# Optimization experiments

Measured on AMD Instinct MI355X. Metric: run time of the kernel, lower is better.

The kernel has to match this reference:

```python
import jax, jax.numpy as jnp
import numpy as np
from jax.scipy.special import gammaln, logsumexp

# Model dims (match init_kwargs)
N1, N2, N3 = 16, 16, 8          # n_state_list
S = N1 * N2 * N3                # tot_dim = 2048 flattened states
M = 16                          # m_dimensions
T = 16384                       # T_max


def setup_inputs() -> dict:
    key = jax.random.key(0)
    ks = jax.random.split(key, 10)
    # observed Poisson counts, shape (T, M)
    x = jax.random.randint(ks[0], (T, M), 0, 20)
    # per-factor Poisson rates: lambda_list[i] = exp(randn(N_i, M)) as in __init__
    lam1 = jnp.exp(jax.random.normal(ks[1], (N1, M), dtype=jnp.float32))
    lam2 = jnp.exp(jax.random.normal(ks[2], (N2, M), dtype=jnp.float32))
    lam3 = jnp.exp(jax.random.normal(ks[3], (N3, M), dtype=jnp.float32))
    # per-factor log transition matrices: softmax over dim 0 (A[next, prev] columns sum to 1)
    logA1 = jax.nn.log_softmax(jax.random.normal(ks[4], (N1, N1), dtype=jnp.float32), axis=0)
    logA2 = jax.nn.log_softmax(jax.random.normal(ks[5], (N2, N2), dtype=jnp.float32), axis=0)
    logA3 = jax.nn.log_softmax(jax.random.normal(ks[6], (N3, N3), dtype=jnp.float32), axis=0)
    # per-factor log state priors: log_softmax(rand(N)*10)
    logpi1 = jax.nn.log_softmax(jax.random.uniform(ks[7], (N1,), dtype=jnp.float32) * 10.0)
    logpi2 = jax.nn.log_softmax(jax.random.uniform(ks[8], (N2,), dtype=jnp.float32) * 10.0)
    logpi3 = jax.nn.log_softmax(jax.random.uniform(ks[9], (N3,), dtype=jnp.float32) * 10.0)
    return {"x": x, "lam1": lam1, "lam2": lam2, "lam3": lam3,
            "logA1": logA1, "logA2": logA2, "logA3": logA3,
            "logpi1": logpi1, "logpi2": logpi2, "logpi3": logpi3}


def reference(x, lam1, lam2, lam3, logA1, logA2, logA3, logpi1, logpi2, logpi3):
    # combine_lambdas: lam_c[s1,s2,s3,m] = lam1[s1,m] + lam2[s2,m] + lam3[s3,m]
    lam_c = (lam1[:, None, None, :] + lam2[None, :, None, :]
             + lam3[None, None, :, :]).reshape(S, M)  # (S, M)
    xf = x.astype(jnp.float32)
    # Poisson log-pmf summed over the M observation dims:
    # em[t, s] = sum_m x[t,m]*log(lam_c[s,m]) - lam_c[s,m] - lgamma(x[t,m]+1)
    em = (xf @ jnp.log(lam_c).T
          - lam_c.sum(axis=-1)[None, :]
          - gammaln(xf + 1.0).sum(axis=-1)[:, None])  # (T, S)
    # combined log transition: logA[dest_flat, prev_flat] = sum_i logA_i[d_i, p_i]
    logA = (logA1[:, None, None, :, None, None]
            + logA2[None, :, None, None, :, None]
            + logA3[None, None, :, None, None, :]).reshape(S, S)
    # combined log priors
    logpi = (logpi1[:, None, None] + logpi2[None, :, None]
             + logpi3[None, None, :]).reshape(S)
    # log-domain forward recurrence (log_alpha_calc)
    alpha0 = em[0] + logpi
    def step(prev, em_t):
        a = em_t + logsumexp(logA + prev[None, :], axis=1)
        return a, None
    alpha_last, _ = jax.lax.scan(step, alpha0, em[1:])
    # log p(x) = logsumexp over final-step alpha
    return logsumexp(alpha_last)
```

## Files before the change

kernel.cpp:

```cpp
#include <hip/hip_runtime.h>
#include <math.h>

#define TMAX 16384
#define MDIM 16
#define SD   2048
#define CLEN 16
#define WUP  8
#define CHKB 512
#define NS   (CLEN + WUP - 1)
#define EROWS 32

typedef unsigned int  uint;
typedef unsigned short ushort;
typedef __attribute__((ext_vector_type(8))) short short8;
typedef __attribute__((ext_vector_type(4))) short short4v;
typedef __attribute__((ext_vector_type(4))) float floatx4;
typedef __attribute__((ext_vector_type(2))) uint uintx2;

template<int CTRL>
__device__ __forceinline__ float fmax_dpp(float v) {
    int o = __builtin_amdgcn_update_dpp(__float_as_int(v), __float_as_int(v),
                                        CTRL, 0xf, 0xf, false);
    return fmaxf(v, __int_as_float(o));
}
__device__ __forceinline__ float waveMax64(float v) {
    v = fmax_dpp<0x111>(v);
    v = fmax_dpp<0x112>(v);
    v = fmax_dpp<0x114>(v);
    v = fmax_dpp<0x118>(v);
    v = fmax_dpp<0x142>(v);
    v = fmax_dpp<0x143>(v);
    return __int_as_float(__builtin_amdgcn_readlane(__float_as_int(v), 63));
}
__device__ __forceinline__ float waveSumF(float v) {
    #pragma unroll
    for (int o = 32; o > 0; o >>= 1) v += __shfl_xor(v, o, 64);
    return v;
}
__device__ __forceinline__ double waveSumD(double v) {
    #pragma unroll
    for (int o = 32; o > 0; o >>= 1) v += __shfl_xor(v, o, 64);
    return v;
}

__device__ __forceinline__ short f2bfs(float f) {
    uint u = __float_as_uint(f);
    return (short)((u + 0x7FFFu + ((u >> 16) & 1u)) >> 16);
}
__device__ __forceinline__ uint pkbf(float a, float b) {
    uint ua = __float_as_uint(a), ub = __float_as_uint(b);
    ua = (ua + 0x7FFFu + ((ua >> 16) & 1u)) >> 16;
    ub = (ub + 0x7FFFu + ((ub >> 16) & 1u)) & 0xFFFF0000u;
    return ua | ub;
}
__device__ __forceinline__ short4v pk4(float a, float b, float c, float d) {
    short4v r;
    r[0] = f2bfs(a); r[1] = f2bfs(b); r[2] = f2bfs(c); r[3] = f2bfs(d);
    return r;
}
__device__ __forceinline__ float bfl(uint u) { return __uint_as_float(u << 16); }
__device__ __forceinline__ float bfh(uint u) { return __uint_as_float(u & 0xFFFF0000u); }

#if __has_builtin(__builtin_amdgcn_mfma_f32_16x16x16bf16_1k)
#define MFMA16(a, b, c) __builtin_amdgcn_mfma_f32_16x16x16bf16_1k(a, b, c, 0, 0, 0)
#else
__device__ __forceinline__ floatx4 mfma16_asm(short4v a, short4v b, floatx4 c) {
    asm volatile("v_mfma_f32_16x16x16_bf16 %0, %1, %2, %0\n\t"
                 "s_nop 7\n\ts_nop 7"
                 : "+v"(c) : "v"(a), "v"(b));
    return c;
}
#define MFMA16(a, b, c) mfma16_asm(a, b, c)
#endif
#define MFMA32(a, b, c) __builtin_amdgcn_mfma_f32_16x16x32_bf16(a, b, c, 0, 0, 0)

__global__ __launch_bounds__(512, 2)
void emP_kernel(const int* __restrict__ x,
                const float* __restrict__ lam1,
                const float* __restrict__ lam2,
                const float* __restrict__ lam3,
                ushort* __restrict__ P,
                float* __restrict__ SumAuxArr,
                float* __restrict__ out) {
    __shared__ float wmx[EROWS][8];
    __shared__ float DemS[EROWS];
    __shared__ float lgtbl[32];
    __shared__ __align__(16) float xfs[EROWS * MDIM];
    __shared__ float lgred;
    const int tid = threadIdx.x, lane = tid & 63, wv = tid >> 6;
    const int q = lane >> 4, nn = lane & 15;
    const int d2 = 2 * wv + (nn >> 3);
    const int d3 = nn & 7;

    if (tid < 32) lgtbl[tid] = lgammaf((float)tid + 1.0f);
    if (tid == 0) lgred = 0.f;

    float llc[4][16], ls[4];
    #pragma unroll
    for (int j = 0; j < 4; ++j) {
        const int d1 = 4 * q + j;
        float sum = 0.f;
        #pragma unroll
        for (int m = 0; m < 16; ++m) {
            float la = lam1[d1 * 16 + m] + lam2[d2 * 16 + m] + lam3[d3 * 16 + m];
            sum += la;
            llc[j][m] = __logf(la);
        }
        ls[j] = sum;
    }

    const int t0 = blockIdx.x * EROWS;
    const int xv = x[t0 * MDIM + tid];
    xfs[tid] = (float)xv;
    __syncthreads();
    {
        double lg = (double)lgtbl[xv & 31];
        lg = waveSumD(lg);
        if (lane == 0) atomicAdd(&lgred, (float)lg);
    }

    float em[EROWS][4];
    #pragma unroll
    for (int ti = 0; ti < EROWS; ++ti) {
        float xr[16];
        *(float4*)&xr[0]  = *(const float4*)&xfs[ti * 16 + 0];
        *(float4*)&xr[4]  = *(const float4*)&xfs[ti * 16 + 4];
        *(float4*)&xr[8]  = *(const float4*)&xfs[ti * 16 + 8];
        *(float4*)&xr[12] = *(const float4*)&xfs[ti * 16 + 12];
        float vm = -3.4e38f;
        #pragma unroll
        for (int j = 0; j < 4; ++j) {
            float d = 0.f;
            #pragma unroll
            for (int m = 0; m < 16; ++m) d = fmaf(xr[m], llc[j][m], d);
            em[ti][j] = d - ls[j];
            vm = fmaxf(vm, em[ti][j]);
        }
        vm = waveMax64(vm);
        if (lane == 0) wmx[ti][wv] = vm;
    }
    __syncthreads();
    if (tid < 32) {
        float m = wmx[tid][0];
        #pragma unroll
        for (int i = 1; i < 8; ++i) m = fmaxf(m, wmx[tid][i]);
        DemS[tid] = m;
    }
    __syncthreads();

    #pragma unroll
    for (int ti = 0; ti < EROWS; ++ti) {
        const float Dem = DemS[ti];
        uint2 w;
        w.x = pkbf(__expf(em[ti][0] - Dem), __expf(em[ti][1] - Dem));
        w.y = pkbf(__expf(em[ti][2] - Dem), __expf(em[ti][3] - Dem));
        *(uint2*)(P + (size_t)(t0 + ti) * SD + tid * 4) = w;
    }

    if (tid == 0) {
        double sumD = 0.0;
        #pragma unroll
        for (int i = 0; i < EROWS; ++i) sumD += (double)DemS[i];
        SumAuxArr[blockIdx.x] = (float)sumD - lgred;
        if (blockIdx.x == 0) out[0] = 0.f;
    }
}

__global__ __launch_bounds__(512, 4)
void fhmm_chunk_kernel(const ushort* __restrict__ P,
                       const float* __restrict__ SumAuxArr,
                       const float* __restrict__ logA1,
                       const float* __restrict__ logA2,
                       const float* __restrict__ logA3,
                       const float* __restrict__ logpi1,
                       const float* __restrict__ logpi2,
                       const float* __restrict__ logpi3,
                       float* __restrict__ out)
{
    __shared__ __align__(16) short c1bA[2 * 2048];
    __shared__ __align__(16) short c1bB[2 * 2048];
    __shared__ float wmAA[8], wmAB[8];
    __shared__ float sred[8];
    __shared__ float saux8[8];

    const int tid  = threadIdx.x;
    const int lane = tid & 63;
    const int wv   = tid >> 6;
    const int q    = lane >> 4;
    const int ml   = lane & 15;

    const int b   = blockIdx.x;
    const int tA0 = (b == 0) ? 0 : 32 * b - WUP;
    const int tB0 = 32 * b + (CLEN - WUP);

    short4v bA1k;
    #pragma unroll
    for (int j = 0; j < 4; ++j)
        bA1k[j] = f2bfs(__expf(logA1[ml * 16 + 4 * q + j]));

    const int d2p = 2 * wv + (ml >> 3);
    const int d3p = ml & 7;
    short8 bK[4];
    #pragma unroll
    for (int jc = 0; jc < 4; ++jc)
        #pragma unroll
        for (int i = 0; i < 8; ++i)
            bK[jc][i] = f2bfs(__expf(logA2[d2p * 16 + 4 * jc + q] + logA3[d3p * 8 + i]));

    const int oS1w = ml * 128 + ((((2 * wv + (q >> 1)) ^ ml) & 15) << 3) + 4 * (q & 1);
    int o23[4];
    #pragma unroll
    for (int jc = 0; jc < 4; ++jc)
        o23[jc] = ml * 128 + ((((4 * jc + q) ^ ml) & 15) << 3);

    if (b == 0) {
        float sx = waveSumF(SumAuxArr[tid]);
        if (lane == 0) saux8[wv] = sx;
    }

    double OFF = 0.0;
    float nuA[4], nuB[4];
    {
        uintx2 p0 = *(const uintx2*)(P + (size_t)tA0 * SD + tid * 4);
        if (b == 0) {
            float lp23 = logpi2[d2p] + logpi3[d3p];
            nuA[0] = bfl(p0.x) * __expf(logpi1[4 * q + 0] + lp23);
            nuA[1] = bfh(p0.x) * __expf(logpi1[4 * q + 1] + lp23);
            nuA[2] = bfl(p0.y) * __expf(logpi1[4 * q + 2] + lp23);
            nuA[3] = bfh(p0.y) * __expf(logpi1[4 * q + 3] + lp23);
        } else {
            nuA[0] = bfl(p0.x); nuA[1] = bfh(p0.x);
            nuA[2] = bfl(p0.y); nuA[3] = bfh(p0.y);
        }
    }
    {
        uintx2 p0 = *(const uintx2*)(P + (size_t)tB0 * SD + tid * 4);
        nuB[0] = bfl(p0.x); nuB[1] = bfh(p0.x);
        nuB[2] = bfl(p0.y); nuB[3] = bfh(p0.y);
    }

    uintx2 PbA0 = *(const uintx2*)(P + (size_t)(tA0 + 1) * SD + tid * 4);
    uintx2 PbA1 = *(const uintx2*)(P + (size_t)(tA0 + 2) * SD + tid * 4);
    uintx2 PbB0 = *(const uintx2*)(P + (size_t)(tB0 + 1) * SD + tid * 4);
    uintx2 PbB1 = *(const uintx2*)(P + (size_t)(tB0 + 2) * SD + tid * 4);

#define SSTEP(S, RESC, ACCFA, ACCFB)                                            \
{                                                                               \
    const int par = (S) & 1;          \
    short* cAq = c1bA + (par << 11);                                            \
    short* cBq = c1bB + (par << 11);                                            \
    {                                 \
        short4v afA = pk4(nuA[0], nuA[1], nuA[2], nuA[3]);                      \
        short4v afB = pk4(nuB[0], nuB[1], nuB[2], nuB[3]);                      \
        floatx4 sA = {0.f, 0.f, 0.f, 0.f};                                      \
        floatx4 sB = {0.f, 0.f, 0.f, 0.f};                                      \
        sA = MFMA16(afA, bA1k, sA);                                             \
        sB = MFMA16(afB, bA1k, sB);                                             \
        ((uintx2*)(cAq + oS1w))[0] = (uintx2){pkbf(sA[0], sA[1]), pkbf(sA[2], sA[3])}; \
        ((uintx2*)(cBq + oS1w))[0] = (uintx2){pkbf(sB[0], sB[1]), pkbf(sB[2], sB[3])}; \
    }                                                                           \
    __syncthreads();                                                            \
    const int tnA = (tA0 + (S) + 2 < TMAX) ? tA0 + (S) + 2 : TMAX - 1;          \
    const int tnB = (tB0 + (S) + 2 < TMAX) ? tB0 + (S) + 2 : TMAX - 1;          \
    uintx2 PbA2 = *(const uintx2*)(P + (size_t)tnA * SD + tid * 4);             \
    uintx2 PbB2 = *(const uintx2*)(P + (size_t)tnB * SD + tid * 4);             \
    float invA = 1.f, invB = 1.f;                                               \
    if (RESC) {                                                                 \
        float mpA = waveMax64(wmAA[lane & 7]);                                  \
        float mpB = waveMax64(wmAB[lane & 7]);                                  \
        float mgA = fmaxf(mpA, 1e-30f);                                         \
        float mgB = fmaxf(mpB, 1e-30f);                                         \
        invA = __builtin_amdgcn_rcpf(mgA);                                      \
        invB = __builtin_amdgcn_rcpf(mgB);                                      \
        if (tid == 0) {                                                         \
            if (ACCFA) OFF += (double)__logf(mgA);                              \
            if (ACCFB) OFF += (double)__logf(mgB);                              \
        }                                                                       \
    }                                                                           \
    {              \
        short8 fA0 = *(const short8*)(cAq + o23[0]);                            \
        short8 fA1 = *(const short8*)(cAq + o23[1]);                            \
        short8 fA2 = *(const short8*)(cAq + o23[2]);                            \
        short8 fA3 = *(const short8*)(cAq + o23[3]);                            \
        short8 fB0 = *(const short8*)(cBq + o23[0]);                            \
        short8 fB1 = *(const short8*)(cBq + o23[1]);                            \
        short8 fB2 = *(const short8*)(cBq + o23[2]);                            \
        short8 fB3 = *(const short8*)(cBq + o23[3]);                            \
        floatx4 aA0 = {0.f, 0.f, 0.f, 0.f};                                     \
        floatx4 aA1 = {0.f, 0.f, 0.f, 0.f};                                     \
        floatx4 aB0 = {0.f, 0.f, 0.f, 0.f};                                     \
        floatx4 aB1 = {0.f, 0.f, 0.f, 0.f};                                     \
        aA0 = MFMA32(fA0, bK[0], aA0);  aB0 = MFMA32(fB0, bK[0], aB0);          \
        aA1 = MFMA32(fA1, bK[1], aA1);  aB1 = MFMA32(fB1, bK[1], aB1);          \
        aA0 = MFMA32(fA2, bK[2], aA0);  aB0 = MFMA32(fB2, bK[2], aB0);          \
        aA1 = MFMA32(fA3, bK[3], aA1);  aB1 = MFMA32(fB3, bK[3], aB1);          \
        floatx4 accA = aA0 + aA1;                                               \
        floatx4 accB = aB0 + aB1;                                               \
        if (RESC) {                                                             \
            nuA[0] = bfl(PbA0.x) * accA[0] * invA;                              \
            nuA[1] = bfh(PbA0.x) * accA[1] * invA;                              \
            nuA[2] = bfl(PbA0.y) * accA[2] * invA;                              \
            nuA[3] = bfh(PbA0.y) * accA[3] * invA;                              \
            nuB[0] = bfl(PbB0.x) * accB[0] * invB;                              \
            nuB[1] = bfh(PbB0.x) * accB[1] * invB;                              \
            nuB[2] = bfl(PbB0.y) * accB[2] * invB;                              \
            nuB[3] = bfh(PbB0.y) * accB[3] * invB;                              \
        } else {                                                                \
            nuA[0] = bfl(PbA0.x) * accA[0];                                     \
            nuA[1] = bfh(PbA0.x) * accA[1];                                     \
            nuA[2] = bfl(PbA0.y) * accA[2];                                     \
            nuA[3] = bfh(PbA0.y) * accA[3];                                     \
            nuB[0] = bfl(PbB0.x) * accB[0];                                     \
            nuB[1] = bfh(PbB0.x) * accB[1];                                     \
            nuB[2] = bfl(PbB0.y) * accB[2];                                     \
            nuB[3] = bfh(PbB0.y) * accB[3];                                     \
            float waA = waveMax64(fmaxf(fmaxf(nuA[0], nuA[1]), fmaxf(nuA[2], nuA[3]))); \
            float waB = waveMax64(fmaxf(fmaxf(nuB[0], nuB[1]), fmaxf(nuB[2], nuB[3]))); \
            if (lane == 0) { wmAA[wv] = waA; wmAB[wv] = waB; }                  \
        }                                                                       \
    }                                                                           \
    PbA0 = PbA1; PbA1 = PbA2; PbB0 = PbB1; PbB1 = PbB2;                         \
}

    SSTEP(1, false, false, false);
    for (int s = 2; s < NS; s += 2) {
        const bool accfA = (b == 0) || (s > WUP);
        const bool accfB = (s > WUP);
        SSTEP(s, true, accfA, accfB);
        SSTEP(s + 1, false, false, false);
    }
#undef SSTEP

    __syncthreads();

    if (b == CHKB - 1) {
        float su = waveSumF(nuB[0] + nuB[1] + nuB[2] + nuB[3]);
        if (lane == 0) sred[wv] = su;
        __syncthreads();
        if (tid == 0) {
            float mpA = wmAA[0];
            #pragma unroll
            for (int i = 1; i < 8; ++i) mpA = fmaxf(mpA, wmAA[i]);
            OFF += (double)__logf(fmaxf(mpA, 1e-30f));
            float tot = 0.f;
            #pragma unroll
            for (int i = 0; i < 8; ++i) tot += sred[i];
            OFF += (double)__logf(tot);
            atomicAdd(out, (float)OFF);
        }
    } else {
        if (tid == 0) {
            float mpA = wmAA[0], mpB = wmAB[0];
            #pragma unroll
            for (int i = 1; i < 8; ++i) {
                mpA = fmaxf(mpA, wmAA[i]);
                mpB = fmaxf(mpB, wmAB[i]);
            }
            OFF += (double)__logf(fmaxf(mpA, 1e-30f));
            OFF += (double)__logf(fmaxf(mpB, 1e-30f));
            if (b == 0) {
                float sa = 0.f;
                #pragma unroll
                for (int i = 0; i < 8; ++i) sa += saux8[i];
                OFF += (double)sa;
            }
            atomicAdd(out, (float)OFF);
        }
    }
}

extern "C" void kernel_launch(void* const* d_in, const int* in_sizes, int n_in,
                              void* d_out, int out_size, void* d_ws, size_t ws_size,
                              hipStream_t stream) {
    const int*   x      = (const int*)  d_in[0];
    const float* lam1   = (const float*)d_in[1];
    const float* lam2   = (const float*)d_in[2];
    const float* lam3   = (const float*)d_in[3];
    const float* logA1  = (const float*)d_in[4];
    const float* logA2  = (const float*)d_in[5];
    const float* logA3  = (const float*)d_in[6];
    const float* logpi1 = (const float*)d_in[7];
    const float* logpi2 = (const float*)d_in[8];
    const float* logpi3 = (const float*)d_in[9];
    float* out = (float*)d_out;

    float*  SumAuxArr = (float*)d_ws;
    ushort* P         = (ushort*)((char*)d_ws + 4096);

    emP_kernel <<<dim3(TMAX / EROWS), dim3(512), 0, stream>>>(
        x, lam1, lam2, lam3, P, SumAuxArr, out);
    fhmm_chunk_kernel<<<dim3(CHKB), dim3(512), 0, stream>>>(
        P, SumAuxArr, logA1, logA2, logA3, logpi1, logpi2, logpi3, out);
}
```

Baseline: 145.5 us.

## Compute emission matrix with bf16 MFMA and stage P writes through LDS

The emission kernel now computes x·log(lambda) with bf16 MFMA instructions, splitting log-lambda into high and low bf16 parts to keep precision, in place of scalar FMA loops. Results are exponentiated, written to a 64KB LDS staging buffer in a permuted layout, then copied out with coalesced 16-byte stores. The forward warmup length WUP is also cut from 8 to 4, which shortens chunk-kernel work but may reduce accuracy of the chunked recurrence. The large LDS buffer limits emP occupancy to one block per CU.

```diff
diff --git a/kernel.cpp b/kernel.cpp
--- a/kernel.cpp
+++ b/kernel.cpp
@@ -5,10 +5,9 @@
 #define MDIM 16
 #define SD   2048
 #define CLEN 16
-#define WUP  8
+#define WUP  4
 #define CHKB 512
 #define NS   (CLEN + WUP - 1)
-#define EROWS 32
 
 typedef unsigned int  uint;
 typedef unsigned short ushort;
@@ -74,7 +73,7 @@
 #endif
 #define MFMA32(a, b, c) __builtin_amdgcn_mfma_f32_16x16x32_bf16(a, b, c, 0, 0, 0)
 
-__global__ __launch_bounds__(512, 2)
+__global__ __launch_bounds__(512, 1)
 void emP_kernel(const int* __restrict__ x,
                 const float* __restrict__ lam1,
                 const float* __restrict__ lam2,
@@ -82,63 +81,80 @@
                 ushort* __restrict__ P,
                 float* __restrict__ SumAuxArr,
                 float* __restrict__ out) {
-    __shared__ float wmx[EROWS][8];
-    __shared__ float DemS[EROWS];
+    __shared__ __align__(16) ushort Pstg[16 * 2048];
+    __shared__ float wmx[32][8];
+    __shared__ float DemS[32];
     __shared__ float lgtbl[32];
-    __shared__ __align__(16) float xfs[EROWS * MDIM];
     __shared__ float lgred;
+
     const int tid = threadIdx.x, lane = tid & 63, wv = tid >> 6;
-    const int q = lane >> 4, nn = lane & 15;
-    const int d2 = 2 * wv + (nn >> 3);
-    const int d3 = nn & 7;
+    const int c = lane & 15;
+    const int g = lane >> 4;
+    const int t0 = blockIdx.x * 32;
 
     if (tid < 32) lgtbl[tid] = lgammaf((float)tid + 1.0f);
     if (tid == 0) lgred = 0.f;
 
-    float llc[4][16], ls[4];
-    #pragma unroll
-    for (int j = 0; j < 4; ++j) {
-        const int d1 = 4 * q + j;
-        float sum = 0.f;
-        #pragma unroll
-        for (int m = 0; m < 16; ++m) {
-            float la = lam1[d1 * 16 + m] + lam2[d2 * 16 + m] + lam3[d3 * 16 + m];
-            sum += la;
-            llc[j][m] = __logf(la);
-        }
-        ls[j] = sum;
-    }
-
-    const int t0 = blockIdx.x * EROWS;
-    const int xv = x[t0 * MDIM + tid];
-    xfs[tid] = (float)xv;
+    short4v aF[2];
+    #pragma unroll
+    for (int h = 0; h < 2; ++h) {
+        int4 xi = *(const int4*)&x[(t0 + h * 16 + c) * MDIM + g * 4];
+        aF[h] = pk4((float)xi.x, (float)xi.y, (float)xi.z, (float)xi.w);
+    }
+    const float4 l3  = *(const float4*)&lam3[(c & 7) * MDIM + g * 4];
+    const float4 l1a = *(const float4*)&lam1[(2 * wv) * MDIM + g * 4];
+    const float4 l1b = *(const float4*)&lam1[(2 * wv + 1) * MDIM + g * 4];
+
     __syncthreads();
     {
+        int xv = x[t0 * MDIM + tid];
         double lg = (double)lgtbl[xv & 31];
         lg = waveSumD(lg);
         if (lane == 0) atomicAdd(&lgred, (float)lg);
     }
 
-    float em[EROWS][4];
-    #pragma unroll
-    for (int ti = 0; ti < EROWS; ++ti) {
-        float xr[16];
-        *(float4*)&xr[0]  = *(const float4*)&xfs[ti * 16 + 0];
-        *(float4*)&xr[4]  = *(const float4*)&xfs[ti * 16 + 4];
-        *(float4*)&xr[8]  = *(const float4*)&xfs[ti * 16 + 8];
-        *(float4*)&xr[12] = *(const float4*)&xfs[ti * 16 + 12];
-        float vm = -3.4e38f;
-        #pragma unroll
-        for (int j = 0; j < 4; ++j) {
-            float d = 0.f;
+    floatx4 em4[2][16];
+    #pragma unroll
+    for (int st = 0; st < 16; ++st) {
+        const int d2 = ((wv << 5) + (st << 1) + (c >> 3)) & 15;
+        const float4 l2 = *(const float4*)&lam2[d2 * MDIM + g * 4];
+        const float4 l1 = (st < 8) ? l1a : l1b;
+        const float la0 = l1.x + l2.x + l3.x;
+        const float la1 = l1.y + l2.y + l3.y;
+        const float la2 = l1.z + l2.z + l3.z;
+        const float la3 = l1.w + l2.w + l3.w;
+        float lsp = la0 + la1 + la2 + la3;
+        lsp += __shfl_xor(lsp, 16, 64);
+        lsp += __shfl_xor(lsp, 32, 64);
+        const float ll0 = __logf(la0), ll1 = __logf(la1);
+        const float ll2 = __logf(la2), ll3 = __logf(la3);
+        short4v bh, bl;
+        bh[0] = f2bfs(ll0); bl[0] = f2bfs(ll0 - bfl((uint)(ushort)bh[0]));
+        bh[1] = f2bfs(ll1); bl[1] = f2bfs(ll1 - bfl((uint)(ushort)bh[1]));
+        bh[2] = f2bfs(ll2); bl[2] = f2bfs(ll2 - bfl((uint)(ushort)bh[2]));
+        bh[3] = f2bfs(ll3); bl[3] = f2bfs(ll3 - bfl((uint)(ushort)bh[3]));
+        #pragma unroll
+        for (int h = 0; h < 2; ++h) {
+            floatx4 acc = {-lsp, -lsp, -lsp, -lsp};
+            acc = MFMA16(aF[h], bh, acc);
+            acc = MFMA16(aF[h], bl, acc);
+            em4[h][st] = acc;
+        }
+    }
+
+    #pragma unroll
+    for (int h = 0; h < 2; ++h)
+        #pragma unroll
+        for (int r = 0; r < 4; ++r) {
+            float m = em4[h][0][r];
             #pragma unroll
-            for (int m = 0; m < 16; ++m) d = fmaf(xr[m], llc[j][m], d);
-            em[ti][j] = d - ls[j];
-            vm = fmaxf(vm, em[ti][j]);
-        }
-        vm = waveMax64(vm);
-        if (lane == 0) wmx[ti][wv] = vm;
-    }
+            for (int st = 1; st < 16; ++st) m = fmaxf(m, em4[h][st][r]);
+            m = fmaxf(m, __shfl_xor(m, 1, 64));
+            m = fmaxf(m, __shfl_xor(m, 2, 64));
+            m = fmaxf(m, __shfl_xor(m, 4, 64));
+            m = fmaxf(m, __shfl_xor(m, 8, 64));
+            if (c == 0) wmx[h * 16 + g * 4 + r][wv] = m;
+        }
     __syncthreads();
     if (tid < 32) {
         float m = wmx[tid][0];
@@ -149,18 +165,34 @@
     __syncthreads();
 
     #pragma unroll
-    for (int ti = 0; ti < EROWS; ++ti) {
-        const float Dem = DemS[ti];
-        uint2 w;
-        w.x = pkbf(__expf(em[ti][0] - Dem), __expf(em[ti][1] - Dem));
-        w.y = pkbf(__expf(em[ti][2] - Dem), __expf(em[ti][3] - Dem));
-        *(uint2*)(P + (size_t)(t0 + ti) * SD + tid * 4) = w;
+    for (int h = 0; h < 2; ++h) {
+        if (h == 1) __syncthreads();
+        float dd[4];
+        #pragma unroll
+        for (int r = 0; r < 4; ++r) dd[r] = DemS[h * 16 + g * 4 + r];
+        #pragma unroll
+        for (int st = 0; st < 16; ++st) {
+            const int d1 = 2 * wv + (st >> 3);
+            const int oidx = (64 * (st & 7) + 16 * (d1 >> 2) + c) * 4 + (d1 & 3);
+            #pragma unroll
+            for (int r = 0; r < 4; ++r) {
+                float p = __expf(em4[h][st][r] - dd[r]);
+                Pstg[(g * 4 + r) * 2048 + oidx] = (ushort)f2bfs(p);
+            }
+        }
+        __syncthreads();
+        #pragma unroll
+        for (int it = 0; it < 8; ++it) {
+            const int flat = it * 512 + tid;
+            uint4 v = ((const uint4*)Pstg)[flat];
+            *(uint4*)(P + (size_t)(t0 + h * 16) * SD + flat * 8) = v;
+        }
     }
 
     if (tid == 0) {
         double sumD = 0.0;
         #pragma unroll
-        for (int i = 0; i < EROWS; ++i) sumD += (double)DemS[i];
+        for (int i = 0; i < 32; ++i) sumD += (double)DemS[i];
         SumAuxArr[blockIdx.x] = (float)sumD - lgred;
         if (blockIdx.x == 0) out[0] = 0.f;
     }
@@ -246,7 +278,7 @@
 
 #define SSTEP(S, RESC, ACCFA, ACCFB)                                            \
 {                                                                               \
-    const int par = (S) & 1;          \
+    const int par = (S) & 1;                                                    \
     short* cAq = c1bA + (par << 11);                                            \
     short* cBq = c1bB + (par << 11);                                            \
     {                                 \
@@ -387,7 +419,7 @@
     float*  SumAuxArr = (float*)d_ws;
     ushort* P         = (ushort*)((char*)d_ws + 4096);
 
-    emP_kernel <<<dim3(TMAX / EROWS), dim3(512), 0, stream>>>(
+    emP_kernel <<<dim3(TMAX / 32), dim3(512), 0, stream>>>(
         x, lam1, lam2, lam3, P, SumAuxArr, out);
     fhmm_chunk_kernel<<<dim3(CHKB), dim3(512), 0, stream>>>(
         P, SumAuxArr, logA1, logA2, logA3, logpi1, logpi2, logpi3, out);
```

Result: faster. 134.4 us (-7.6%).
